# Performance work log

Measured on AMD Instinct MI355X. Metric: run time of the kernel, lower is better.

Reference implementation:

```python
import jax, jax.numpy as jnp
import numpy as np

B, S, HID = 2, 2048, 4096
H, KVH, D = 32, 8, 128
EPS = 1e-6
BASE = 1000000.0


def _rmsnorm(x, w, eps=EPS):
    # x: [..., D]; RMSNorm over last dim with learned scale
    return x * jax.lax.rsqrt(jnp.mean(x * x, axis=-1, keepdims=True) + eps) * w


def _rope_interleaved(x, cos, sin):
    # x: [B, S, h, D]; cos/sin: [S, D//2]; is_neox_style=False (GPT-J interleaved pairs)
    x1 = x[..., 0::2]
    x2 = x[..., 1::2]
    c = cos[None, :, None, :]
    s = sin[None, :, None, :]
    o1 = x1 * c - x2 * s
    o2 = x2 * c + x1 * s
    return jnp.stack([o1, o2], axis=-1).reshape(x.shape)


def setup_inputs() -> dict:
    key = jax.random.key(0)
    ks = jax.random.split(key, 6)
    scale = 0.02
    return {
        "positions": jnp.arange(S, dtype=jnp.int32),
        "hidden_states": jax.random.normal(ks[0], (B, S, HID), jnp.float32),
        "Wq": jax.random.normal(ks[1], (HID, H * D), jnp.float32) * scale,
        "Wk": jax.random.normal(ks[2], (HID, KVH * D), jnp.float32) * scale,
        "Wv": jax.random.normal(ks[3], (HID, KVH * D), jnp.float32) * scale,
        "Wo": jax.random.normal(ks[4], (H * D, HID), jnp.float32) * scale,
        "q_norm_w": jnp.ones((D,), jnp.float32),
        "k_norm_w": jnp.ones((D,), jnp.float32),
    }


def reference(positions, hidden_states, Wq, Wk, Wv, Wo, q_norm_w, k_norm_w):
    # QKV projections (no bias)
    q = hidden_states @ Wq            # [B,S,H*D]
    k = hidden_states @ Wk            # [B,S,KVH*D]
    v = hidden_states @ Wv            # [B,S,KVH*D]

    # per-head QK RMSNorm
    q = _rmsnorm(q.reshape(B, S, H, D), q_norm_w)
    k = _rmsnorm(k.reshape(B, S, KVH, D), k_norm_w)
    v = v.reshape(B, S, KVH, D)

    # RoPE (non-neox / interleaved), rotary_dim == head_dim
    inv_freq = BASE ** (-jnp.arange(0, D, 2, dtype=jnp.float32) / D)  # [D/2]
    freqs = positions.astype(jnp.float32)[:, None] * inv_freq[None, :]  # [S, D/2]
    cos, sin = jnp.cos(freqs), jnp.sin(freqs)
    q = _rope_interleaved(q, cos, sin)
    k = _rope_interleaved(k, cos, sin)

    # GQA causal attention (prefill path of RadixAttention)
    rep = H // KVH
    kr = jnp.repeat(k, rep, axis=2)   # [B,S,H,D]
    vr = jnp.repeat(v, rep, axis=2)
    scores = jnp.einsum("bqhd,bkhd->bhqk", q, kr) * (D ** -0.5)
    causal = jnp.tril(jnp.ones((S, S), dtype=bool))
    scores = jnp.where(causal[None, None], scores, jnp.float32(-1e30))
    probs = jax.nn.softmax(scores, axis=-1)
    attn = jnp.einsum("bhqk,bkhd->bqhd", probs, vr).reshape(B, S, H * D)

    out = attn @ Wo                   # [B,S,HID]
    return out, k.reshape(B, S, KVH * D), v.reshape(B, S, KVH * D)
```

## Files before the change

### kernel.cpp

```cpp
#include <hip/hip_runtime.h>
#include <math.h>

#define B_SZ 2
#define S_LEN 2048
#define HID_D 4096
#define NH 32
#define NKV 8
#define HD 128
#define NTOK (B_SZ * S_LEN)

typedef short bf16x8 __attribute__((ext_vector_type(8)));
typedef float f32x4 __attribute__((ext_vector_type(4)));

__device__ inline unsigned short bf_rn(float f) {
    unsigned int u = __builtin_bit_cast(unsigned int, f);
    return (unsigned short)((u + 0x7FFFu + ((u >> 16) & 1u)) >> 16);
}
__device__ inline float bf_up(unsigned short s) {
    return __builtin_bit_cast(float, (unsigned int)s << 16);
}

__device__ inline void gload_lds16(const void* g, void* l) {
    __builtin_amdgcn_global_load_lds(
        (const __attribute__((address_space(1))) unsigned int*)g,
        (__attribute__((address_space(3))) unsigned int*)l, 16, 0, 0);
}

__global__ __launch_bounds__(64) void rope_table_kernel(const int* __restrict__ pos,
                                                        float* __restrict__ cosT,
                                                        float* __restrict__ sinT) {
    int s = blockIdx.x;
    int i = threadIdx.x;
    float p = (float)pos[s];
    float inv = expf((float)i * (-13.815510557964274f / 64.0f));
    float f = p * inv;
    cosT[s * 64 + i] = cosf(f);
    sinT[s * 64 + i] = sinf(f);
}

__global__ __launch_bounds__(256) void castv_kernel(const float* __restrict__ src,
                                                    unsigned short* __restrict__ dst,
                                                    int nquads) {
    int i = blockIdx.x * 256 + threadIdx.x;
    if (i >= nquads) return;
    float4 v = ((const float4*)src)[i];
    ushort4 o;
    o.x = bf_rn(v.x); o.y = bf_rn(v.y); o.z = bf_rn(v.z); o.w = bf_rn(v.w);
    ((ushort4*)dst)[i] = o;
}

__global__ __launch_bounds__(256) void cast_t_kernel(const float* __restrict__ src,
                                                     unsigned short* __restrict__ dst,
                                                     int K, int N) {
    __shared__ float tile[32][33];
    const int j0 = blockIdx.x << 5;
    const int i0 = blockIdx.y << 5;
    const int tx = threadIdx.x & 31, ty = threadIdx.x >> 5;
#pragma unroll
    for (int r = 0; r < 32; r += 8)
        tile[ty + r][tx] = src[(size_t)(i0 + ty + r) * N + j0 + tx];
    __syncthreads();
#pragma unroll
    for (int r = 0; r < 32; r += 8)
        dst[(size_t)(j0 + ty + r) * K + i0 + tx] = bf_rn(tile[tx][ty + r]);
}

__global__ __launch_bounds__(256) void vtrans_kernel(const float* __restrict__ vout,
                                                     unsigned short* __restrict__ vtb) {
    __shared__ float tile[32][33];
    const int bh = blockIdx.z;
    const int s0 = blockIdx.x << 5;
    const int d0 = blockIdx.y << 5;
    const int b = bh >> 3, kvh = bh & 7;
    const int tx = threadIdx.x & 31, ty = threadIdx.x >> 5;
#pragma unroll
    for (int r = 0; r < 32; r += 8)
        tile[ty + r][tx] = vout[((size_t)(b * S_LEN + s0 + ty + r) * NKV + kvh) * HD + d0 + tx];
    __syncthreads();
#pragma unroll
    for (int r = 0; r < 32; r += 8)
        vtb[((size_t)(b * NKV + kvh) * HD + d0 + ty + r) * S_LEN + s0 + tx] = bf_rn(tile[tx][ty + r]);
}

template <typename OUT>
__global__ __launch_bounds__(256) void gemm_bt_kernel(const unsigned short* __restrict__ A,
                                                      const unsigned short* __restrict__ Bt,
                                                      OUT* __restrict__ C,
                                                      int M, int N, int K) {
    __shared__ unsigned short As[128 * 32];
    __shared__ unsigned short Bs[128 * 32];
    const int t = threadIdx.x;
    const int lane = t & 63, w = t >> 6;
    const int wr = w >> 1, wc = w & 1;
    const int bm = blockIdx.y << 7, bn = blockIdx.x << 7;

    const int srow = w * 32 + (lane >> 2);
    const int skoff = (lane & 3) << 3;
    const unsigned short* aA0 = A + (size_t)(bm + srow) * K + skoff;
    const unsigned short* aA1 = aA0 + (size_t)16 * K;
    const unsigned short* aB0 = Bt + (size_t)(bn + srow) * K + skoff;
    const unsigned short* aB1 = aB0 + (size_t)16 * K;
    unsigned short* lA0 = As + (w * 2 + 0) * 512;
    unsigned short* lA1 = As + (w * 2 + 1) * 512;
    unsigned short* lB0 = Bs + (w * 2 + 0) * 512;
    unsigned short* lB1 = Bs + (w * 2 + 1) * 512;

    const int fr = lane & 15, fg = lane >> 4;
    const unsigned short* Asp = As + (wr * 64 + fr) * 32 + fg * 8;
    const unsigned short* Bsp = Bs + (wc * 64 + fr) * 32 + fg * 8;

    f32x4 acc[4][4];
#pragma unroll
    for (int m = 0; m < 4; ++m)
#pragma unroll
        for (int n = 0; n < 4; ++n) acc[m][n] = (f32x4)(0.0f);

    const int nk = K >> 5;
    for (int kc = 0; kc < nk; ++kc) {
        __syncthreads();
        const size_t go = (size_t)kc * 32;
        gload_lds16(aA0 + go, lA0);
        gload_lds16(aA1 + go, lA1);
        gload_lds16(aB0 + go, lB0);
        gload_lds16(aB1 + go, lB1);
        __syncthreads();

        bf16x8 af[4], bfr[4];
#pragma unroll
        for (int m = 0; m < 4; ++m) af[m] = *(const bf16x8*)(Asp + m * 512);
#pragma unroll
        for (int n = 0; n < 4; ++n) bfr[n] = *(const bf16x8*)(Bsp + n * 512);
#pragma unroll
        for (int m = 0; m < 4; ++m)
#pragma unroll
            for (int n = 0; n < 4; ++n)
                acc[m][n] = __builtin_amdgcn_mfma_f32_16x16x32_bf16(af[m], bfr[n], acc[m][n], 0, 0, 0);
    }

    const int crow = (lane >> 4) << 2, ccol = lane & 15;
#pragma unroll
    for (int m = 0; m < 4; ++m)
#pragma unroll
        for (int n = 0; n < 4; ++n) {
            OUT* Cp = C + (size_t)(bm + wr * 64 + m * 16 + crow) * N + bn + wc * 64 + n * 16 + ccol;
#pragma unroll
            for (int r = 0; r < 4; ++r) {
                float v = acc[m][n][r];
                if constexpr (sizeof(OUT) == 2) Cp[(size_t)r * N] = bf_rn(v);
                else                            Cp[(size_t)r * N] = v;
            }
        }
}

__global__ __launch_bounds__(64) void norm_rope_kernel(float* __restrict__ buf,
                                                       const float* __restrict__ w,
                                                       const float* __restrict__ cosT,
                                                       const float* __restrict__ sinT,
                                                       int nh) {
    int bid = blockIdx.x;
    int token = bid / nh;
    int h = bid - token * nh;
    int pos = token & (S_LEN - 1);
    int i = threadIdx.x;
    size_t base = (size_t)token * (nh * HD) + (size_t)h * HD + 2 * i;
    float2 x = *(const float2*)(buf + base);
    float ss = x.x * x.x + x.y * x.y;
#pragma unroll
    for (int off = 32; off > 0; off >>= 1) ss += __shfl_xor(ss, off);
    float rn = 1.0f / sqrtf(ss * (1.0f / 128.0f) + 1e-6f);
    float2 wv = *(const float2*)(w + 2 * i);
    float x1 = x.x * rn * wv.x;
    float x2 = x.y * rn * wv.y;
    float c = cosT[pos * 64 + i];
    float sn = sinT[pos * 64 + i];
    float2 o;
    o.x = x1 * c - x2 * sn;
    o.y = x2 * c + x1 * sn;
    *(float2*)(buf + base) = o;
}

__global__ __launch_bounds__(64) void norm_rope_bf16_kernel(unsigned short* __restrict__ buf,
                                                            const float* __restrict__ w,
                                                            const float* __restrict__ cosT,
                                                            const float* __restrict__ sinT,
                                                            int nh) {
    int bid = blockIdx.x;
    int token = bid / nh;
    int h = bid - token * nh;
    int pos = token & (S_LEN - 1);
    int i = threadIdx.x;
    size_t base = (size_t)token * (nh * HD) + (size_t)h * HD + 2 * i;
    unsigned int u = *(const unsigned int*)(buf + base);
    float x1 = bf_up((unsigned short)(u & 0xFFFFu));
    float x2 = bf_up((unsigned short)(u >> 16));
    float ss = x1 * x1 + x2 * x2;
#pragma unroll
    for (int off = 32; off > 0; off >>= 1) ss += __shfl_xor(ss, off);
    float rn = 1.0f / sqrtf(ss * (1.0f / 128.0f) + 1e-6f);
    float2 wv = *(const float2*)(w + 2 * i);
    x1 *= rn * wv.x;
    x2 *= rn * wv.y;
    float c = cosT[pos * 64 + i];
    float sn = sinT[pos * 64 + i];
    float o1 = x1 * c - x2 * sn;
    float o2 = x2 * c + x1 * sn;
    unsigned int ou = (unsigned int)bf_rn(o1) | ((unsigned int)bf_rn(o2) << 16);
    *(unsigned int*)(buf + base) = ou;
}

#define PADQ 136
#define PADV 72

__global__ __launch_bounds__(256, 4) void attn_mfma_kernel(const unsigned short* __restrict__ Qb,
                                                           const float* __restrict__ Kf,
                                                           const unsigned short* __restrict__ Vb,
                                                           unsigned short* __restrict__ O) {
    __shared__ unsigned short Ks[64 * PADQ];
    __shared__ unsigned short Ps[64 * PADV];
    const int t = threadIdx.x;
    const int lane = t & 63, w = t >> 6;
    const int c = lane & 15, g = lane >> 4;
    const int qt = blockIdx.x, h = blockIdx.y, b = blockIdx.z;
    const int kvh = h >> 2;
    const size_t tok0 = (size_t)b * S_LEN + (size_t)qt * 64;
    const size_t vbase = ((size_t)(b * NKV + kvh)) * HD * S_LEN;

    bf16x8 qf[4];
    {
        const unsigned short* qrow = Qb + (tok0 + w * 16 + c) * HID_D + (size_t)h * HD;
#pragma unroll
        for (int ks = 0; ks < 4; ++ks) qf[ks] = *(const bf16x8*)(qrow + ks * 32 + g * 8);
    }

    f32x4 o[8];
#pragma unroll
    for (int dt = 0; dt < 8; ++dt) o[dt] = (f32x4)(0.0f);
    float mrow[4], lrow[4];
#pragma unroll
    for (int r = 0; r < 4; ++r) { mrow[r] = -INFINITY; lrow[r] = 0.0f; }
    const float sc = 0.12751743f;

    const int kr_ = t >> 2, kc0 = (t & 3) * 32;

    for (int kt = 0; kt <= qt; ++kt) {
        {
            const size_t gb = ((size_t)b * S_LEN + (size_t)kt * 64 + kr_) * (NKV * HD) + (size_t)kvh * HD + kc0;
            unsigned short* kd = Ks + kr_ * PADQ + kc0;
#pragma unroll
            for (int j = 0; j < 8; ++j) {
                float4 v = *(const float4*)(Kf + gb + j * 4);
                ushort4 o4;
                o4.x = bf_rn(v.x); o4.y = bf_rn(v.y);
                o4.z = bf_rn(v.z); o4.w = bf_rn(v.w);
                *(ushort4*)(kd + j * 4) = o4;
            }
        }
        __syncthreads();

        f32x4 s[4];
#pragma unroll
        for (int ct = 0; ct < 4; ++ct) s[ct] = (f32x4)(0.0f);
#pragma unroll
        for (int ks = 0; ks < 4; ++ks) {
            bf16x8 kf[4];
#pragma unroll
            for (int ct = 0; ct < 4; ++ct)
                kf[ct] = *(const bf16x8*)(Ks + (ct * 16 + c) * PADQ + ks * 32 + g * 8);
#pragma unroll
            for (int ct = 0; ct < 4; ++ct)
                s[ct] = __builtin_amdgcn_mfma_f32_16x16x32_bf16(qf[ks], kf[ct], s[ct], 0, 0, 0);
        }
        __syncthreads();

        const int rowbase = qt * 64 + w * 16 + g * 4;
        const int colbase = kt * 64 + c;
#pragma unroll
        for (int r = 0; r < 4; ++r) {
            float v0 = s[0][r] * sc, v1 = s[1][r] * sc, v2 = s[2][r] * sc, v3 = s[3][r] * sc;
            if (kt == qt) {
                const int rq = rowbase + r;
                if (colbase + 0  > rq) v0 = -1e30f;
                if (colbase + 16 > rq) v1 = -1e30f;
                if (colbase + 32 > rq) v2 = -1e30f;
                if (colbase + 48 > rq) v3 = -1e30f;
            }
            float mx = fmaxf(fmaxf(v0, v1), fmaxf(v2, v3));
#pragma unroll
            for (int off = 8; off > 0; off >>= 1) mx = fmaxf(mx, __shfl_xor(mx, off));
            const float mn = fmaxf(mrow[r], mx);
            const float sf = exp2f(mrow[r] - mn);
            mrow[r] = mn;
            const float p0 = exp2f(v0 - mn), p1 = exp2f(v1 - mn);
            const float p2 = exp2f(v2 - mn), p3 = exp2f(v3 - mn);
            unsigned short* pr = Ps + (w * 16 + g * 4 + r) * PADV + c;
            pr[0]  = bf_rn(p0);
            pr[16] = bf_rn(p1);
            pr[32] = bf_rn(p2);
            pr[48] = bf_rn(p3);
            float rs = p0 + p1 + p2 + p3;
#pragma unroll
            for (int off = 8; off > 0; off >>= 1) rs += __shfl_xor(rs, off);
            lrow[r] = lrow[r] * sf + rs;
#pragma unroll
            for (int dt = 0; dt < 8; ++dt) o[dt][r] *= sf;
        }

        const unsigned short* vt0 = Vb + vbase + (size_t)kt * 64 + g * 8;
#pragma unroll
        for (int ks = 0; ks < 2; ++ks) {
            bf16x8 pf = *(const bf16x8*)(Ps + (w * 16 + c) * PADV + ks * 32 + g * 8);
#pragma unroll
            for (int dt = 0; dt < 8; ++dt) {
                bf16x8 vf = *(const bf16x8*)(vt0 + (size_t)(dt * 16 + c) * S_LEN + ks * 32);
                o[dt] = __builtin_amdgcn_mfma_f32_16x16x32_bf16(pf, vf, o[dt], 0, 0, 0);
            }
        }
    }

#pragma unroll
    for (int r = 0; r < 4; ++r) {
        const float inv = 1.0f / lrow[r];
        const size_t rowoff = (tok0 + w * 16 + g * 4 + r) * HID_D + (size_t)h * HD;
#pragma unroll
        for (int dt = 0; dt < 8; ++dt)
            O[rowoff + dt * 16 + c] = bf_rn(o[dt][r] * inv);
    }
}

extern "C" void kernel_launch(void* const* d_in, const int* in_sizes, int n_in,
                              void* d_out, int out_size, void* d_ws, size_t ws_size,
                              hipStream_t stream) {
    const int* positions = (const int*)d_in[0];
    const float* hidden  = (const float*)d_in[1];
    const float* Wq      = (const float*)d_in[2];
    const float* Wk      = (const float*)d_in[3];
    const float* Wv      = (const float*)d_in[4];
    const float* Wo      = (const float*)d_in[5];
    const float* qw      = (const float*)d_in[6];
    const float* kw      = (const float*)d_in[7];

    float* out  = (float*)d_out;
    float* kout = out + (size_t)NTOK * HID_D;
    float* vout = kout + (size_t)NTOK * NKV * HD;

    char* w8 = (char*)d_ws;
    float* cosT = (float*)w8;
    float* sinT = cosT + S_LEN * 64;
    unsigned short* qbuf = (unsigned short*)(sinT + S_LEN * 64);
    unsigned short* hb   = qbuf + (size_t)NTOK * HID_D;
    unsigned short* Wt   = hb + (size_t)NTOK * HID_D;
    unsigned short* vtb  = Wt + (size_t)HID_D * HID_D;
    unsigned short* ab   = hb;

    rope_table_kernel<<<S_LEN, 64, 0, stream>>>(positions, cosT, sinT);
    castv_kernel<<<(NTOK * HID_D / 4 + 255) / 256, 256, 0, stream>>>(hidden, hb, NTOK * HID_D / 4);

    cast_t_kernel<<<dim3(NKV * HD / 32, HID_D / 32), 256, 0, stream>>>(Wk, Wt, HID_D, NKV * HD);
    gemm_bt_kernel<float><<<dim3(NKV * HD / 128, NTOK / 128), 256, 0, stream>>>(hb, Wt, kout, NTOK, NKV * HD, HID_D);
    cast_t_kernel<<<dim3(NKV * HD / 32, HID_D / 32), 256, 0, stream>>>(Wv, Wt, HID_D, NKV * HD);
    gemm_bt_kernel<float><<<dim3(NKV * HD / 128, NTOK / 128), 256, 0, stream>>>(hb, Wt, vout, NTOK, NKV * HD, HID_D);
    vtrans_kernel<<<dim3(S_LEN / 32, HD / 32, B_SZ * NKV), 256, 0, stream>>>(vout, vtb);
    cast_t_kernel<<<dim3(HID_D / 32, HID_D / 32), 256, 0, stream>>>(Wq, Wt, HID_D, HID_D);
    gemm_bt_kernel<unsigned short><<<dim3(HID_D / 128, NTOK / 128), 256, 0, stream>>>(hb, Wt, qbuf, NTOK, HID_D, HID_D);
    cast_t_kernel<<<dim3(HID_D / 32, HID_D / 32), 256, 0, stream>>>(Wo, Wt, HID_D, HID_D);

    norm_rope_bf16_kernel<<<NTOK * NH, 64, 0, stream>>>(qbuf, qw, cosT, sinT, NH);
    norm_rope_kernel<<<NTOK * NKV, 64, 0, stream>>>(kout, kw, cosT, sinT, NKV);

    attn_mfma_kernel<<<dim3(S_LEN / 64, NH, B_SZ), 256, 0, stream>>>(qbuf, kout, vtb, ab);

    gemm_bt_kernel<float><<<dim3(HID_D / 128, NTOK / 128), 256, 0, stream>>>(ab, Wt, out, NTOK, HID_D, HID_D);
}
```

Before: 1.569 ms.

## Prefetch K/V tiles into registers and stage V through LDS in attention

The norm-rope kernel now also writes a bf16 copy of K in a head-major layout, so the attention kernel can load ready-to-use bf16 K tiles instead of converting fp32 K on every tile. The next K and V tiles are loaded into registers while the current tile is being computed, and V is staged through shared memory instead of being read straight from global memory inside the MFMA loop. One of the two syncthreads per iteration is dropped. The cost is extra LDS and registers, which may lower occupancy, plus an extra bf16 K write. The bf16 K path runs only when the workspace is large enough.

```diff
diff --git a/kernel.cpp b/kernel.cpp
--- a/kernel.cpp
+++ b/kernel.cpp
@@ -156,7 +156,8 @@
                                                        const float* __restrict__ w,
                                                        const float* __restrict__ cosT,
                                                        const float* __restrict__ sinT,
-                                                       int nh) {
+                                                       int nh,
+                                                       unsigned int* __restrict__ kb16u) {
     int bid = blockIdx.x;
     int token = bid / nh;
     int h = bid - token * nh;
@@ -177,6 +178,12 @@
     o.x = x1 * c - x2 * sn;
     o.y = x2 * c + x1 * sn;
     *(float2*)(buf + base) = o;
+    if (kb16u) {
+        int b = token >> 11;
+        int s = token & (S_LEN - 1);
+        unsigned int pk = (unsigned int)bf_rn(o.x) | ((unsigned int)bf_rn(o.y) << 16);
+        kb16u[(((size_t)b * NKV + h) * S_LEN + s) * 64 + i] = pk;
+    }
 }
 
 __global__ __launch_bounds__(64) void norm_rope_bf16_kernel(unsigned short* __restrict__ buf,
@@ -211,11 +218,14 @@
 #define PADQ 136
 #define PADV 72
 
+template <int KMODE>
 __global__ __launch_bounds__(256, 4) void attn_mfma_kernel(const unsigned short* __restrict__ Qb,
                                                            const float* __restrict__ Kf,
+                                                           const unsigned short* __restrict__ Kb16,
                                                            const unsigned short* __restrict__ Vb,
                                                            unsigned short* __restrict__ O) {
     __shared__ unsigned short Ks[64 * PADQ];
+    __shared__ unsigned short Vt[128 * PADV];
     __shared__ unsigned short Ps[64 * PADV];
     const int t = threadIdx.x;
     const int lane = t & 63, w = t >> 6;
@@ -224,6 +234,7 @@
     const int kvh = h >> 2;
     const size_t tok0 = (size_t)b * S_LEN + (size_t)qt * 64;
     const size_t vbase = ((size_t)(b * NKV + kvh)) * HD * S_LEN;
+    const size_t kbbase = ((size_t)(b * NKV + kvh)) * S_LEN * HD;
 
     bf16x8 qf[4];
     {
@@ -232,6 +243,21 @@
         for (int ks = 0; ks < 4; ++ks) qf[ks] = *(const bf16x8*)(qrow + ks * 32 + g * 8);
     }
 
+    const int vr = t >> 3, vc8 = (t & 7) * 8;
+    const int kr_ = t >> 2, kc0 = (t & 3) * 32;
+    uint4 vreg[4], kreg[4];
+    {
+        const unsigned short* vsrc = Vb + vbase + vc8;
+#pragma unroll
+        for (int pp = 0; pp < 4; ++pp)
+            vreg[pp] = *(const uint4*)(vsrc + (size_t)(vr + pp * 32) * S_LEN);
+        if constexpr (KMODE == 0) {
+            const unsigned short* kb = Kb16 + kbbase + (size_t)kr_ * HD + kc0;
+#pragma unroll
+            for (int j = 0; j < 4; ++j) kreg[j] = *(const uint4*)(kb + j * 8);
+        }
+    }
+
     f32x4 o[8];
 #pragma unroll
     for (int dt = 0; dt < 8; ++dt) o[dt] = (f32x4)(0.0f);
@@ -240,10 +266,18 @@
     for (int r = 0; r < 4; ++r) { mrow[r] = -INFINITY; lrow[r] = 0.0f; }
     const float sc = 0.12751743f;
 
-    const int kr_ = t >> 2, kc0 = (t & 3) * 32;
-
     for (int kt = 0; kt <= qt; ++kt) {
-        {
+        __syncthreads();
+
+#pragma unroll
+        for (int pp = 0; pp < 4; ++pp)
+            *(uint4*)(Vt + (vr + pp * 32) * PADV + vc8) = vreg[pp];
+
+        if constexpr (KMODE == 0) {
+            unsigned short* kd = Ks + kr_ * PADQ + kc0;
+#pragma unroll
+            for (int j = 0; j < 4; ++j) *(uint4*)(kd + j * 8) = kreg[j];
+        } else {
             const size_t gb = ((size_t)b * S_LEN + (size_t)kt * 64 + kr_) * (NKV * HD) + (size_t)kvh * HD + kc0;
             unsigned short* kd = Ks + kr_ * PADQ + kc0;
 #pragma unroll
@@ -257,6 +291,18 @@
         }
         __syncthreads();
 
+        if (kt < qt) {
+            const unsigned short* vsrc = Vb + vbase + (size_t)(kt + 1) * 64 + vc8;
+#pragma unroll
+            for (int pp = 0; pp < 4; ++pp)
+                vreg[pp] = *(const uint4*)(vsrc + (size_t)(vr + pp * 32) * S_LEN);
+            if constexpr (KMODE == 0) {
+                const unsigned short* kb = Kb16 + kbbase + ((size_t)(kt + 1) * 64 + kr_) * HD + kc0;
+#pragma unroll
+                for (int j = 0; j < 4; ++j) kreg[j] = *(const uint4*)(kb + j * 8);
+            }
+        }
+
         f32x4 s[4];
 #pragma unroll
         for (int ct = 0; ct < 4; ++ct) s[ct] = (f32x4)(0.0f);
@@ -270,7 +316,6 @@
             for (int ct = 0; ct < 4; ++ct)
                 s[ct] = __builtin_amdgcn_mfma_f32_16x16x32_bf16(qf[ks], kf[ct], s[ct], 0, 0, 0);
         }
-        __syncthreads();
 
         const int rowbase = qt * 64 + w * 16 + g * 4;
         const int colbase = kt * 64 + c;
@@ -305,13 +350,12 @@
             for (int dt = 0; dt < 8; ++dt) o[dt][r] *= sf;
         }
 
-        const unsigned short* vt0 = Vb + vbase + (size_t)kt * 64 + g * 8;
 #pragma unroll
         for (int ks = 0; ks < 2; ++ks) {
             bf16x8 pf = *(const bf16x8*)(Ps + (w * 16 + c) * PADV + ks * 32 + g * 8);
 #pragma unroll
             for (int dt = 0; dt < 8; ++dt) {
-                bf16x8 vf = *(const bf16x8*)(vt0 + (size_t)(dt * 16 + c) * S_LEN + ks * 32);
+                bf16x8 vf = *(const bf16x8*)(Vt + (dt * 16 + c) * PADV + ks * 32 + g * 8);
                 o[dt] = __builtin_amdgcn_mfma_f32_16x16x32_bf16(pf, vf, o[dt], 0, 0, 0);
             }
         }
@@ -350,7 +394,11 @@
     unsigned short* hb   = qbuf + (size_t)NTOK * HID_D;
     unsigned short* Wt   = hb + (size_t)NTOK * HID_D;
     unsigned short* vtb  = Wt + (size_t)HID_D * HID_D;
+    unsigned short* kb16 = vtb + (size_t)B_SZ * NKV * HD * S_LEN;
     unsigned short* ab   = hb;
+
+    const size_t need_kb16 = (size_t)((char*)(kb16 + (size_t)B_SZ * NKV * S_LEN * HD) - w8);
+    const bool use_kb16 = ws_size >= need_kb16;
 
     rope_table_kernel<<<S_LEN, 64, 0, stream>>>(positions, cosT, sinT);
     castv_kernel<<<(NTOK * HID_D / 4 + 255) / 256, 256, 0, stream>>>(hidden, hb, NTOK * HID_D / 4);
@@ -365,9 +413,13 @@
     cast_t_kernel<<<dim3(HID_D / 32, HID_D / 32), 256, 0, stream>>>(Wo, Wt, HID_D, HID_D);
 
     norm_rope_bf16_kernel<<<NTOK * NH, 64, 0, stream>>>(qbuf, qw, cosT, sinT, NH);
-    norm_rope_kernel<<<NTOK * NKV, 64, 0, stream>>>(kout, kw, cosT, sinT, NKV);
-
-    attn_mfma_kernel<<<dim3(S_LEN / 64, NH, B_SZ), 256, 0, stream>>>(qbuf, kout, vtb, ab);
+    norm_rope_kernel<<<NTOK * NKV, 64, 0, stream>>>(kout, kw, cosT, sinT, NKV,
+                                                    use_kb16 ? (unsigned int*)kb16 : nullptr);
+
+    if (use_kb16)
+        attn_mfma_kernel<0><<<dim3(S_LEN / 64, NH, B_SZ), 256, 0, stream>>>(qbuf, kout, kb16, vtb, ab);
+    else
+        attn_mfma_kernel<1><<<dim3(S_LEN / 64, NH, B_SZ), 256, 0, stream>>>(qbuf, kout, kb16, vtb, ab);
 
     gemm_bt_kernel<float><<<dim3(HID_D / 128, NTOK / 128), 256, 0, stream>>>(ab, Wt, out, NTOK, HID_D, HID_D);
 }
```

Result: faster. 1.497 ms (-4.6%).
